# Performance work log

Hardware: AMD Instinct MI355X
Metric: run time of the kernel (lower is better)

## Reference

```python
import jax, jax.numpy as jnp
import numpy as np
import math

DIM = 1024
NUMHEADS = 16
HEAD_DIM = DIM // NUMHEADS
B, N = 4, 1024


def setup_inputs() -> dict:
    key = jax.random.key(0)
    ks = jax.random.split(key, 12)
    x = jax.random.normal(ks[0], (B, N, DIM), dtype=jnp.float32)
    decaymask = jax.random.uniform(ks[1], (NUMHEADS, N, N), dtype=jnp.float32)
    s = 1.0 / math.sqrt(DIM)
    wq = jax.random.normal(ks[2], (DIM, DIM), dtype=jnp.float32) * s
    bq = jnp.zeros((DIM,), dtype=jnp.float32)
    wk = jax.random.normal(ks[3], (DIM, DIM), dtype=jnp.float32) * s
    bk = jnp.zeros((DIM,), dtype=jnp.float32)
    wv = jax.random.normal(ks[4], (DIM, DIM), dtype=jnp.float32) * s
    bv = jnp.zeros((DIM,), dtype=jnp.float32)
    wo = jax.random.normal(ks[5], (DIM, DIM), dtype=jnp.float32) * s
    bo = jnp.zeros((DIM,), dtype=jnp.float32)
    return {"x": x, "decaymask": decaymask, "wq": wq, "bq": bq, "wk": wk,
            "bk": bk, "wv": wv, "bv": bv, "wo": wo, "bo": bo}


def reference(x, decaymask, wq, bq, wk, bk, wv, bv, wo, bo):
    Bx, Nx, D = x.shape
    # projections (torch Linear: x @ W^T + b)
    q = x @ wq.T + bq
    k = x @ wk.T + bk
    v = x @ wv.T + bv
    # [B, H, N, Hd]
    q = q.reshape(Bx, Nx, NUMHEADS, HEAD_DIM).transpose(0, 2, 1, 3)
    k = k.reshape(Bx, Nx, NUMHEADS, HEAD_DIM).transpose(0, 2, 1, 3)
    v = v.reshape(Bx, Nx, NUMHEADS, HEAD_DIM).transpose(0, 2, 1, 3)
    scores = jnp.einsum('bhqd,bhkd->bhqk', q, k) / math.sqrt(HEAD_DIM)
    scores = scores * decaymask[None]  # multiplicative decay mask before softmax
    attn = jax.nn.softmax(scores, axis=-1)
    out = jnp.einsum('bhqk,bhkd->bhqd', attn, v)
    out = out.transpose(0, 2, 1, 3).reshape(Bx, Nx, D)
    return out @ wo.T + bo
```

## Files before the change

### kernel.cpp

```cpp
#include <hip/hip_runtime.h>
#include <hip/hip_bf16.h>
#include <math.h>

typedef __bf16 bf16;
typedef __bf16 bf16x8 __attribute__((ext_vector_type(8)));
typedef __bf16 bf16x4 __attribute__((ext_vector_type(4)));
typedef float f32x4 __attribute__((ext_vector_type(4)));
typedef unsigned short u16;
typedef u16 u16x8 __attribute__((ext_vector_type(8)));

#define SEQ 1024
#define DIMSZ 1024
#define NHEADS 16
#define HEADDIM 64
#define BATCH 4
#define MTOK (BATCH * SEQ)

#define QSCALE 0.180336880f

typedef __attribute__((address_space(1))) const unsigned char gas_u8;
typedef __attribute__((address_space(3))) unsigned char las_u8;
__device__ __forceinline__ void gload16(const void* g, void* l) {
    __builtin_amdgcn_global_load_lds((const gas_u8*)g, (las_u8*)l, 16, 0, 0);
}

__device__ __forceinline__ void cvt_store(const float4 v, bf16* dst, int e0, float scale) {
    int row = e0 >> 10, col = e0 & 1023;
    int col2 = (col & ~63) | (col & 7) | (((((col >> 3) & 7) ^ (row & 7))) << 3);
    bf16x4 o;
    o[0] = (bf16)(v.x * scale);
    o[1] = (bf16)(v.y * scale);
    o[2] = (bf16)(v.z * scale);
    o[3] = (bf16)(v.w * scale);
    *reinterpret_cast<bf16x4*>(&dst[(size_t)row * 1024 + col2]) = o;
}

__global__ void cvt_all(const float4* __restrict__ x,
                        const float4* __restrict__ wq, const float4* __restrict__ wk,
                        const float4* __restrict__ wv, const float4* __restrict__ wo,
                        bf16* __restrict__ xb, bf16* __restrict__ wqkvb,
                        bf16* __restrict__ wob) {
    int i = blockIdx.x * blockDim.x + threadIdx.x;
    if (i < 1048576) {
        cvt_store(x[i], xb, i << 2, 1.f);
    } else {
        int li = i - 1048576;
        int mat = li >> 18, lj = li & 262143;
        const float4* s = (mat == 0) ? wq : (mat == 1) ? wk : (mat == 2) ? wv : wo;
        bf16* d = (mat < 3) ? (wqkvb + (size_t)mat * 1024 * 1024) : wob;
        cvt_store(s[lj], d, lj << 2, (mat == 0) ? QSCALE : 1.f);
    }
}

__device__ __forceinline__ bf16x8 fragswz(const bf16* base, int row, int kb) {
    return *reinterpret_cast<const bf16x8*>(
        reinterpret_cast<const char*>(base) + row * 128 + (kb ^ ((row & 7) << 4)));
}

#define LDT 72

template <int WN, int OUT_F32>
__global__ __launch_bounds__(256) void gemm_glds(
    const bf16* __restrict__ A, const bf16* __restrict__ Bm,
    const float* __restrict__ b0, const float* __restrict__ b1, const float* __restrict__ b2,
    float s0, void* __restrict__ Cv, int M, int N, int K)
{
    __shared__ __align__(16) bf16 As[128 * 64];
    __shared__ __align__(16) bf16 Bs[WN * 32 * 64];

    const int BN = WN * 32;
    const int nbn = N / BN;
    const int wrk = (blockIdx.x & 7) * ((int)gridDim.x >> 3) + (blockIdx.x >> 3);
    const int bm = wrk / nbn, bn = wrk % nbn;
    const int m0 = bm << 7, n0 = bn * BN;
    const int tid = threadIdx.x, lane = tid & 63, wid = tid >> 6;
    const int wr = wid >> 1, wc = wid & 1;
    const int lq = lane & 15, g = lane >> 4;

    f32x4 acc[4][WN];
    #pragma unroll
    for (int m = 0; m < 4; ++m)
        #pragma unroll
        for (int n = 0; n < WN; ++n)
            acc[m][n] = (f32x4){0.f, 0.f, 0.f, 0.f};

    for (int kt = 0; kt < K; kt += 64) {
        #pragma unroll
        for (int i = 0; i < 4; ++i) {
            int rb = wid * 32 + i * 8;
            gload16(&A[(size_t)(m0 + rb + (lane >> 3)) * K + kt + ((lane & 7) << 3)],
                    &As[rb * 64]);
        }
        #pragma unroll
        for (int i = 0; i < WN; ++i) {
            int rb = wid * (WN * 8) + i * 8;
            gload16(&Bm[(size_t)(n0 + rb + (lane >> 3)) * K + kt + ((lane & 7) << 3)],
                    &Bs[rb * 64]);
        }
        __syncthreads();

        bf16x8 af[4][2], bfr[WN][2];
        #pragma unroll
        for (int m = 0; m < 4; ++m)
            #pragma unroll
            for (int h2 = 0; h2 < 2; ++h2)
                af[m][h2] = fragswz(As, wr * 64 + m * 16 + lq, h2 * 64 + g * 16);
        #pragma unroll
        for (int n = 0; n < WN; ++n)
            #pragma unroll
            for (int h2 = 0; h2 < 2; ++h2)
                bfr[n][h2] = fragswz(Bs, wc * (WN * 16) + n * 16 + lq, h2 * 64 + g * 16);

        #pragma unroll
        for (int m = 0; m < 4; ++m)
            #pragma unroll
            for (int n = 0; n < WN; ++n)
                #pragma unroll
                for (int h2 = 0; h2 < 2; ++h2)
                    acc[m][n] = __builtin_amdgcn_mfma_f32_16x16x32_bf16(
                        af[m][h2], bfr[n][h2], acc[m][n], 0, 0, 0);
        __syncthreads();
    }

    const int seg = n0 >> 10;
    const float* bp = (seg == 0) ? b0 : ((seg == 1) ? b1 : b2);
    const float bsc = (seg == 0) ? s0 : 1.f;

    #pragma unroll
    for (int m = 0; m < 4; ++m) {
        #pragma unroll
        for (int n = 0; n < WN; ++n) {
            int rbase = m0 + wr * 64 + m * 16 + (g << 2);
            int col = n0 + wc * (WN * 16) + n * 16 + lq;
            float bv = bp[col - (seg << 10)] * bsc;
            #pragma unroll
            for (int r = 0; r < 4; ++r) {
                float v = acc[m][n][r] + bv;
                if (OUT_F32)
                    ((float*)Cv)[(size_t)(rbase + r) * N + col] = v;
                else
                    ((bf16*)Cv)[(size_t)(rbase + r) * N + col] = (bf16)v;
            }
        }
    }
}

struct KV { bf16x8 a, b; };

__device__ __forceinline__ void issue_kv(KV& r, const bf16* qkv, int brow,
                                         int koff, int voff, int tid) {
    if (tid < 256) {
        const int rK = tid >> 3, o8 = (tid & 7) << 3;
        r.a = *reinterpret_cast<const bf16x8*>(&qkv[(size_t)(brow + rK) * 3072 + koff + o8]);
        r.b = *reinterpret_cast<const bf16x8*>(&qkv[(size_t)(brow + rK + 32) * 3072 + koff + o8]);
    } else {
        const int t2 = tid - 256;
        const int kp = t2 >> 3, o8 = (t2 & 7) << 3;
        r.a = *reinterpret_cast<const bf16x8*>(&qkv[(size_t)(brow + 2 * kp) * 3072 + voff + o8]);
        r.b = *reinterpret_cast<const bf16x8*>(&qkv[(size_t)(brow + 2 * kp + 1) * 3072 + voff + o8]);
    }
}

__device__ __forceinline__ void write_kv(const KV& r, bf16* Kb, bf16* Vb, int tid) {
    if (tid < 256) {
        const int rK = tid >> 3, o = tid & 7;
        char* kb = reinterpret_cast<char*>(Kb);
        int kx = (o << 4) ^ ((rK & 7) << 4);
        *reinterpret_cast<bf16x8*>(kb + rK * 128 + kx) = r.a;
        *reinterpret_cast<bf16x8*>(kb + (rK + 32) * 128 + kx) = r.b;
    } else {
        const int t2 = tid - 256;
        const int kp = t2 >> 3, o = t2 & 7;
        const u16x8 v0 = *reinterpret_cast<const u16x8*>(&r.a);
        const u16x8 v1 = *reinterpret_cast<const u16x8*>(&r.b);
        char* vb = reinterpret_cast<char*>(Vb);
        #pragma unroll
        for (int j = 0; j < 8; ++j) {
            int d = (o << 3) + j;
            int byteo = (d * 144 + kp * 4) ^ (o << 4);
            unsigned int w = (unsigned int)v0[j] | ((unsigned int)v1[j] << 16);
            *reinterpret_cast<unsigned int*>(vb + byteo) = w;
        }
    }
}

__device__ __forceinline__ void compute_stage(
    const bf16* Kb, const bf16* Vb, bf16* Psw,
    const float4 (&mreg)[4], const bf16x8 (&aqb)[2],
    f32x4& lacc, f32x4 (&oacc)[4], int lane)
{
    const int lq = lane & 15, g = lane >> 4;
    f32x4 sacc[4];
    #pragma unroll
    for (int ct = 0; ct < 4; ++ct) sacc[ct] = (f32x4){0.f, 0.f, 0.f, 0.f};
    #pragma unroll
    for (int ct = 0; ct < 4; ++ct)
        #pragma unroll
        for (int h2 = 0; h2 < 2; ++h2)
            sacc[ct] = __builtin_amdgcn_mfma_f32_16x16x32_bf16(
                fragswz(Kb, ct * 16 + lq, h2 * 64 + g * 16), aqb[h2], sacc[ct], 0, 0, 0);

    #pragma unroll
    for (int ct = 0; ct < 4; ++ct) {
        float p0 = __builtin_exp2f(sacc[ct][0] * mreg[ct].x);
        float p1 = __builtin_exp2f(sacc[ct][1] * mreg[ct].y);
        float p2 = __builtin_exp2f(sacc[ct][2] * mreg[ct].z);
        float p3 = __builtin_exp2f(sacc[ct][3] * mreg[ct].w);
        lacc[0] += p0; lacc[1] += p1; lacc[2] += p2; lacc[3] += p3;
        bf16x4 pbv;
        pbv[0] = (bf16)p0; pbv[1] = (bf16)p1; pbv[2] = (bf16)p2; pbv[3] = (bf16)p3;
        *reinterpret_cast<bf16x4*>(&Psw[lq * LDT + ct * 16 + (g << 2)]) = pbv;
    }

    const char* vb = reinterpret_cast<const char*>(Vb);
    #pragma unroll
    for (int ot = 0; ot < 4; ++ot) {
        #pragma unroll
        for (int h2 = 0; h2 < 2; ++h2) {
            int d = ot * 16 + lq;
            int byteo = (d * 144 + (h2 * 32 + g * 8) * 2) ^ (((d >> 3) & 7) << 4);
            bf16x8 vf = *reinterpret_cast<const bf16x8*>(vb + byteo);
            bf16x8 pf = *reinterpret_cast<const bf16x8*>(&Psw[lq * LDT + h2 * 32 + g * 8]);
            oacc[ot] = __builtin_amdgcn_mfma_f32_16x16x32_bf16(vf, pf, oacc[ot], 0, 0, 0);
        }
    }
}

__global__ __launch_bounds__(512, 4) void attn_kernel(
    const bf16* __restrict__ qkv, const float* __restrict__ mask, bf16* __restrict__ Og)
{
    __shared__ __align__(16) bf16 Kbuf[2][64 * 64];
    __shared__ __align__(16) bf16 Vbuf[2][64 * LDT];
    __shared__ __align__(16) bf16 Ps[8][16 * LDT];

    const int bid = blockIdx.x;
    const int xcd = bid & 7, slot = bid >> 3;
    const int b = slot & 3;
    const int pg = xcd * 16 + (slot >> 2);
    const int h = pg >> 3, qblk = pg & 7;

    const int tid = threadIdx.x, lane = tid & 63, wid = tid >> 6;
    const int lq = lane & 15, g = lane >> 4;
    const int q = (qblk << 7) + wid * 16 + lq;
    const int brow = b * SEQ;
    const int koff = 1024 + h * HEADDIM, voff = 2048 + h * HEADDIM, qoff = h * HEADDIM;
    const float* mh = mask + (size_t)h * SEQ * SEQ + (size_t)q * SEQ;

    bf16x8 aq[2];
    #pragma unroll
    for (int h2 = 0; h2 < 2; ++h2)
        aq[h2] = *reinterpret_cast<const bf16x8*>(
            &qkv[(size_t)(brow + q) * 3072 + qoff + h2 * 32 + g * 8]);

    f32x4 lacc = {};
    f32x4 oacc[4] = {};

    KV s;
    issue_kv(s, qkv, brow, koff, voff, tid);
    write_kv(s, Kbuf[0], Vbuf[0], tid);
    issue_kv(s, qkv, brow + 64, koff, voff, tid);
    float4 mcur[4], mnxt[4];
    #pragma unroll
    for (int ct = 0; ct < 4; ++ct)
        mcur[ct] = *reinterpret_cast<const float4*>(&mh[ct * 16 + (g << 2)]);
    __syncthreads();

    for (int t = 0; t < 16; ++t) {
        int pp = t & 1, np = pp ^ 1;
        if (t < 15) write_kv(s, Kbuf[np], Vbuf[np], tid);
        if (t < 14) issue_kv(s, qkv, brow + (t + 2) * 64, koff, voff, tid);
        if (t < 15)
            #pragma unroll
            for (int ct = 0; ct < 4; ++ct)
                mnxt[ct] = *reinterpret_cast<const float4*>(&mh[(t + 1) * 64 + ct * 16 + (g << 2)]);
        compute_stage(Kbuf[pp], Vbuf[pp], Ps[wid], mcur, aq, lacc, oacc, lane);
        if (t < 15)
            #pragma unroll
            for (int ct = 0; ct < 4; ++ct) mcur[ct] = mnxt[ct];
        __syncthreads();
    }

    float lsum = lacc[0] + lacc[1] + lacc[2] + lacc[3];
    lsum += __shfl_xor(lsum, 16, 64);
    lsum += __shfl_xor(lsum, 32, 64);
    float inv = 1.f / lsum;
    #pragma unroll
    for (int ot = 0; ot < 4; ++ot) {
        bf16x4 o;
        o[0] = (bf16)(oacc[ot][0] * inv);
        o[1] = (bf16)(oacc[ot][1] * inv);
        o[2] = (bf16)(oacc[ot][2] * inv);
        o[3] = (bf16)(oacc[ot][3] * inv);
        int lcol = ot * 16 + (g << 2);
        int chunk = (lcol >> 3) ^ (q & 7);
        int col = h * HEADDIM + (chunk << 3) + (lcol & 7);
        *reinterpret_cast<bf16x4*>(&Og[(size_t)(brow + q) * DIMSZ + col]) = o;
    }
}

extern "C" void kernel_launch(void* const* d_in, const int* in_sizes, int n_in,
                              void* d_out, int out_size, void* d_ws, size_t ws_size,
                              hipStream_t stream) {
    const float* x    = (const float*)d_in[0];
    const float* mask = (const float*)d_in[1];
    const float* wq   = (const float*)d_in[2];
    const float* bq   = (const float*)d_in[3];
    const float* wk   = (const float*)d_in[4];
    const float* bk   = (const float*)d_in[5];
    const float* wv   = (const float*)d_in[6];
    const float* bv   = (const float*)d_in[7];
    const float* wo   = (const float*)d_in[8];
    const float* bo   = (const float*)d_in[9];
    float* out = (float*)d_out;

    char* ws = (char*)d_ws;
    bf16* xb    = (bf16*)ws; ws += (size_t)MTOK * DIMSZ * 2;
    bf16* wqkvb = (bf16*)ws; ws += (size_t)3 * DIMSZ * DIMSZ * 2;
    bf16* wob   = (bf16*)ws; ws += (size_t)DIMSZ * DIMSZ * 2;
    bf16* qkv   = (bf16*)ws; ws += (size_t)MTOK * 3 * DIMSZ * 2;
    bf16* aob   = (bf16*)ws; ws += (size_t)MTOK * DIMSZ * 2;

    cvt_all<<<(2 * 1048576) / 256, 256, 0, stream>>>(
        (const float4*)x, (const float4*)wq, (const float4*)wk,
        (const float4*)wv, (const float4*)wo, xb, wqkvb, wob);

    gemm_glds<4, 0><<<(MTOK / 128) * (3 * DIMSZ / 128), 256, 0, stream>>>(
        xb, wqkvb, bq, bk, bv, QSCALE, qkv, MTOK, 3 * DIMSZ, DIMSZ);

    attn_kernel<<<512, 512, 0, stream>>>(qkv, mask, aob);

    gemm_glds<2, 1><<<(MTOK / 128) * (DIMSZ / 64), 256, 0, stream>>>(
        aob, wob, bo, bo, bo, 1.f, out, MTOK, DIMSZ, DIMSZ);
}
```

Baseline: 105.6 us.

## Split attention key dimension across wave pairs and double grid size

Each attention block now covers 64 queries instead of 128. Its 8 waves split into two groups that each handle half of every 64-key tile, and the partial outputs and row sums are combined through shared memory at the end. The grid doubles to 1024 blocks and the launch-bounds occupancy hint rises to 6, so more work is spread across the CUs. In exchange, each K/V tile is loaded once per 64 queries instead of once per 128, doubling K/V global and LDS traffic, and the final merge adds a barrier.

```diff
diff --git a/kernel.cpp b/kernel.cpp
--- a/kernel.cpp
+++ b/kernel.cpp
@@ -184,49 +184,7 @@
     }
 }
 
-__device__ __forceinline__ void compute_stage(
-    const bf16* Kb, const bf16* Vb, bf16* Psw,
-    const float4 (&mreg)[4], const bf16x8 (&aqb)[2],
-    f32x4& lacc, f32x4 (&oacc)[4], int lane)
-{
-    const int lq = lane & 15, g = lane >> 4;
-    f32x4 sacc[4];
-    #pragma unroll
-    for (int ct = 0; ct < 4; ++ct) sacc[ct] = (f32x4){0.f, 0.f, 0.f, 0.f};
-    #pragma unroll
-    for (int ct = 0; ct < 4; ++ct)
-        #pragma unroll
-        for (int h2 = 0; h2 < 2; ++h2)
-            sacc[ct] = __builtin_amdgcn_mfma_f32_16x16x32_bf16(
-                fragswz(Kb, ct * 16 + lq, h2 * 64 + g * 16), aqb[h2], sacc[ct], 0, 0, 0);
-
-    #pragma unroll
-    for (int ct = 0; ct < 4; ++ct) {
-        float p0 = __builtin_exp2f(sacc[ct][0] * mreg[ct].x);
-        float p1 = __builtin_exp2f(sacc[ct][1] * mreg[ct].y);
-        float p2 = __builtin_exp2f(sacc[ct][2] * mreg[ct].z);
-        float p3 = __builtin_exp2f(sacc[ct][3] * mreg[ct].w);
-        lacc[0] += p0; lacc[1] += p1; lacc[2] += p2; lacc[3] += p3;
-        bf16x4 pbv;
-        pbv[0] = (bf16)p0; pbv[1] = (bf16)p1; pbv[2] = (bf16)p2; pbv[3] = (bf16)p3;
-        *reinterpret_cast<bf16x4*>(&Psw[lq * LDT + ct * 16 + (g << 2)]) = pbv;
-    }
-
-    const char* vb = reinterpret_cast<const char*>(Vb);
-    #pragma unroll
-    for (int ot = 0; ot < 4; ++ot) {
-        #pragma unroll
-        for (int h2 = 0; h2 < 2; ++h2) {
-            int d = ot * 16 + lq;
-            int byteo = (d * 144 + (h2 * 32 + g * 8) * 2) ^ (((d >> 3) & 7) << 4);
-            bf16x8 vf = *reinterpret_cast<const bf16x8*>(vb + byteo);
-            bf16x8 pf = *reinterpret_cast<const bf16x8*>(&Psw[lq * LDT + h2 * 32 + g * 8]);
-            oacc[ot] = __builtin_amdgcn_mfma_f32_16x16x32_bf16(vf, pf, oacc[ot], 0, 0, 0);
-        }
-    }
-}
-
-__global__ __launch_bounds__(512, 4) void attn_kernel(
+__global__ __launch_bounds__(512, 6) void attn_kernel(
     const bf16* __restrict__ qkv, const float* __restrict__ mask, bf16* __restrict__ Og)
 {
     __shared__ __align__(16) bf16 Kbuf[2][64 * 64];
@@ -236,15 +194,16 @@
     const int bid = blockIdx.x;
     const int xcd = bid & 7, slot = bid >> 3;
     const int b = slot & 3;
-    const int pg = xcd * 16 + (slot >> 2);
-    const int h = pg >> 3, qblk = pg & 7;
+    const int pg = xcd * 32 + (slot >> 2);
+    const int h = pg >> 4, qblk = pg & 15;
 
     const int tid = threadIdx.x, lane = tid & 63, wid = tid >> 6;
+    const int kh = wid >> 2, qw = wid & 3;
     const int lq = lane & 15, g = lane >> 4;
-    const int q = (qblk << 7) + wid * 16 + lq;
+    const int q = (qblk << 6) + qw * 16 + lq;
     const int brow = b * SEQ;
     const int koff = 1024 + h * HEADDIM, voff = 2048 + h * HEADDIM, qoff = h * HEADDIM;
-    const float* mh = mask + (size_t)h * SEQ * SEQ + (size_t)q * SEQ;
+    const float* mh = mask + (size_t)h * SEQ * SEQ + (size_t)q * SEQ + kh * 32;
 
     bf16x8 aq[2];
     #pragma unroll
@@ -259,10 +218,10 @@
     issue_kv(s, qkv, brow, koff, voff, tid);
     write_kv(s, Kbuf[0], Vbuf[0], tid);
     issue_kv(s, qkv, brow + 64, koff, voff, tid);
-    float4 mcur[4], mnxt[4];
+    float4 mcur[2], mnxt[2];
     #pragma unroll
-    for (int ct = 0; ct < 4; ++ct)
-        mcur[ct] = *reinterpret_cast<const float4*>(&mh[ct * 16 + (g << 2)]);
+    for (int c = 0; c < 2; ++c)
+        mcur[c] = *reinterpret_cast<const float4*>(&mh[c * 16 + (g << 2)]);
     __syncthreads();
 
     for (int t = 0; t < 16; ++t) {
@@ -271,30 +230,80 @@
         if (t < 14) issue_kv(s, qkv, brow + (t + 2) * 64, koff, voff, tid);
         if (t < 15)
             #pragma unroll
-            for (int ct = 0; ct < 4; ++ct)
-                mnxt[ct] = *reinterpret_cast<const float4*>(&mh[(t + 1) * 64 + ct * 16 + (g << 2)]);
-        compute_stage(Kbuf[pp], Vbuf[pp], Ps[wid], mcur, aq, lacc, oacc, lane);
+            for (int c = 0; c < 2; ++c)
+                mnxt[c] = *reinterpret_cast<const float4*>(&mh[(t + 1) * 64 + c * 16 + (g << 2)]);
+
+        {
+            const bf16* Kb = Kbuf[pp];
+            const char* vb = reinterpret_cast<const char*>(Vbuf[pp]);
+            bf16* Psw = Ps[wid];
+            f32x4 sacc[2];
+            #pragma unroll
+            for (int c = 0; c < 2; ++c) sacc[c] = (f32x4){0.f, 0.f, 0.f, 0.f};
+            #pragma unroll
+            for (int c = 0; c < 2; ++c)
+                #pragma unroll
+                for (int h2 = 0; h2 < 2; ++h2)
+                    sacc[c] = __builtin_amdgcn_mfma_f32_16x16x32_bf16(
+                        fragswz(Kb, (2 * kh + c) * 16 + lq, h2 * 64 + g * 16),
+                        aq[h2], sacc[c], 0, 0, 0);
+
+            #pragma unroll
+            for (int c = 0; c < 2; ++c) {
+                float p0 = __builtin_exp2f(sacc[c][0] * mcur[c].x);
+                float p1 = __builtin_exp2f(sacc[c][1] * mcur[c].y);
+                float p2 = __builtin_exp2f(sacc[c][2] * mcur[c].z);
+                float p3 = __builtin_exp2f(sacc[c][3] * mcur[c].w);
+                lacc[0] += p0; lacc[1] += p1; lacc[2] += p2; lacc[3] += p3;
+                bf16x4 pbv;
+                pbv[0] = (bf16)p0; pbv[1] = (bf16)p1; pbv[2] = (bf16)p2; pbv[3] = (bf16)p3;
+                *reinterpret_cast<bf16x4*>(&Psw[lq * LDT + c * 16 + (g << 2)]) = pbv;
+            }
+
+            bf16x8 pf = *reinterpret_cast<const bf16x8*>(&Psw[lq * LDT + g * 8]);
+            #pragma unroll
+            for (int ot = 0; ot < 4; ++ot) {
+                int d = ot * 16 + lq;
+                int byteo = (d * 144 + (kh * 32 + g * 8) * 2) ^ (((d >> 3) & 7) << 4);
+                bf16x8 vf = *reinterpret_cast<const bf16x8*>(vb + byteo);
+                oacc[ot] = __builtin_amdgcn_mfma_f32_16x16x32_bf16(vf, pf, oacc[ot], 0, 0, 0);
+            }
+        }
+
         if (t < 15)
             #pragma unroll
-            for (int ct = 0; ct < 4; ++ct) mcur[ct] = mnxt[ct];
+            for (int c = 0; c < 2; ++c) mcur[c] = mnxt[c];
         __syncthreads();
     }
 
     float lsum = lacc[0] + lacc[1] + lacc[2] + lacc[3];
     lsum += __shfl_xor(lsum, 16, 64);
     lsum += __shfl_xor(lsum, 32, 64);
-    float inv = 1.f / lsum;
-    #pragma unroll
-    for (int ot = 0; ot < 4; ++ot) {
-        bf16x4 o;
-        o[0] = (bf16)(oacc[ot][0] * inv);
-        o[1] = (bf16)(oacc[ot][1] * inv);
-        o[2] = (bf16)(oacc[ot][2] * inv);
-        o[3] = (bf16)(oacc[ot][3] * inv);
-        int lcol = ot * 16 + (g << 2);
-        int chunk = (lcol >> 3) ^ (q & 7);
-        int col = h * HEADDIM + (chunk << 3) + (lcol & 7);
-        *reinterpret_cast<bf16x4*>(&Og[(size_t)(brow + q) * DIMSZ + col]) = o;
+
+    f32x4* cO = reinterpret_cast<f32x4*>(Vbuf);
+    float* cl = reinterpret_cast<float*>(Kbuf);
+    if (kh == 1) {
+        #pragma unroll
+        for (int ot = 0; ot < 4; ++ot)
+            cO[ot * 256 + qw * 64 + lane] = oacc[ot];
+        cl[qw * 64 + lane] = lsum;
+    }
+    __syncthreads();
+    if (kh == 0) {
+        float inv = 1.f / (lsum + cl[qw * 64 + lane]);
+        #pragma unroll
+        for (int ot = 0; ot < 4; ++ot) {
+            f32x4 o2 = cO[ot * 256 + qw * 64 + lane];
+            bf16x4 o;
+            o[0] = (bf16)((oacc[ot][0] + o2[0]) * inv);
+            o[1] = (bf16)((oacc[ot][1] + o2[1]) * inv);
+            o[2] = (bf16)((oacc[ot][2] + o2[2]) * inv);
+            o[3] = (bf16)((oacc[ot][3] + o2[3]) * inv);
+            int lcol = ot * 16 + (g << 2);
+            int chunk = (lcol >> 3) ^ (q & 7);
+            int col = h * HEADDIM + (chunk << 3) + (lcol & 7);
+            *reinterpret_cast<bf16x4*>(&Og[(size_t)(brow + q) * DIMSZ + col]) = o;
+        }
     }
 }
 
@@ -327,7 +336,7 @@
     gemm_glds<4, 0><<<(MTOK / 128) * (3 * DIMSZ / 128), 256, 0, stream>>>(
         xb, wqkvb, bq, bk, bv, QSCALE, qkv, MTOK, 3 * DIMSZ, DIMSZ);
 
-    attn_kernel<<<512, 512, 0, stream>>>(qkv, mask, aob);
+    attn_kernel<<<1024, 512, 0, stream>>>(qkv, mask, aob);
 
     gemm_glds<2, 1><<<(MTOK / 128) * (DIMSZ / 64), 256, 0, stream>>>(
         aob, wob, bo, bo, bo, 1.f, out, MTOK, DIMSZ, DIMSZ);
```

Measured after the change: 112.4 us. 1.06x slower.
